# Kernel optimization log

Hardware: AMD Instinct MI355X
Metric: run time of the kernel (lower is better)

Reference implementation:

```python
import jax, jax.numpy as jnp
import numpy as np

N_NODES = 100000
N_EDGES = 600000
F_IN = 128
HIDDEN = 128
Z_DIM = 64


def setup_inputs() -> dict:
    key = jax.random.key(0)
    ks = jax.random.split(key, 8)
    nodes = jax.random.normal(ks[0], (N_NODES, F_IN), dtype=jnp.float32)
    senders = jax.random.randint(ks[1], (N_EDGES,), 0, N_NODES, dtype=jnp.int32)
    receivers = jax.random.randint(ks[2], (N_EDGES,), 0, N_NODES, dtype=jnp.int32)
    s = lambda fan_in: 1.0 / np.sqrt(fan_in)
    W0 = jax.random.normal(ks[3], (F_IN, HIDDEN), dtype=jnp.float32) * s(F_IN)
    b0 = jnp.zeros((HIDDEN,), dtype=jnp.float32)
    W1 = jax.random.normal(ks[4], (HIDDEN, HIDDEN), dtype=jnp.float32) * s(HIDDEN)
    b1 = jnp.zeros((HIDDEN,), dtype=jnp.float32)
    Wmu = jax.random.normal(ks[5], (HIDDEN + F_IN, Z_DIM), dtype=jnp.float32) * s(HIDDEN + F_IN)
    bmu = jnp.zeros((Z_DIM,), dtype=jnp.float32)
    Wls = jax.random.normal(ks[6], (HIDDEN + F_IN, Z_DIM), dtype=jnp.float32) * s(HIDDEN + F_IN)
    bls = jnp.zeros((Z_DIM,), dtype=jnp.float32)
    return dict(nodes=nodes, senders=senders, receivers=receivers,
                W0=W0, b0=b0, W1=W1, b1=b1, Wmu=Wmu, bmu=bmu, Wls=Wls, bls=bls)


def _gc_layer(h, senders, receivers, W, b):
    """jraph.GraphConvolution with symmetric normalization, no self edges.
    update_node_fn = softmax(relu(Dense(h)))."""
    n = h.shape[0]
    h = jax.nn.softmax(jax.nn.relu(h @ W + b), axis=-1)  # [N, H]
    ones = jnp.ones_like(senders, dtype=h.dtype)
    sender_deg = jax.ops.segment_sum(ones, senders, num_segments=n)    # [N]
    receiver_deg = jax.ops.segment_sum(ones, receivers, num_segments=n)
    h = h * jax.lax.rsqrt(jnp.maximum(sender_deg, 1.0))[:, None]
    h = jax.ops.segment_sum(h[senders], receivers, num_segments=n)     # scatter-aggregate
    h = h * jax.lax.rsqrt(jnp.maximum(receiver_deg, 1.0))[:, None]
    return h


def reference(nodes, senders, receivers, W0, b0, W1, b1, Wmu, bmu, Wls, bls):
    h = _gc_layer(nodes, senders, receivers, W0, b0)
    h = _gc_layer(h, senders, receivers, W1, b1)
    h = jnp.concatenate([h, nodes], axis=-1)  # [N, HIDDEN + F_IN]
    mu = h @ Wmu + bmu
    logsig2 = h @ Wls + bls
    return (mu, logsig2)
```

## Files before the change

kernel.cpp:

```cpp
#include <hip/hip_runtime.h>

#define N_NODES 100000
#define N_EDGES 600000

#define NBUCK 391
#define BROWS 512
#define NCHUNK 128
#define V4_TOTAL (N_EDGES / 4)
#define V4_CHUNK ((V4_TOTAL + NCHUNK - 1) / NCHUNK)

typedef __attribute__((ext_vector_type(8))) short short8;
typedef __attribute__((ext_vector_type(4))) float f32x4;

__device__ inline unsigned short bf16r(float x) {
    unsigned u = __float_as_uint(x);
    return (unsigned short)((u + 0x7FFFu + ((u >> 16) & 1u)) >> 16);
}
__device__ inline unsigned bf16pack2(float x, float y) {
    unsigned ux = __float_as_uint(x), uy = __float_as_uint(y);
    ux = (ux + 0x7FFFu + ((ux >> 16) & 1u)) >> 16;
    uy = (uy + 0x7FFFu + ((uy >> 16) & 1u)) >> 16;
    return ux | (uy << 16);
}

__global__ void prep_weights(const float* __restrict__ W0, const float* __restrict__ W1,
                             const float* __restrict__ Wmu, const float* __restrict__ Wls,
                             unsigned short* __restrict__ w0t, unsigned short* __restrict__ w1t,
                             unsigned short* __restrict__ wht) {
    int i = blockIdx.x * 256 + threadIdx.x;
    if (i < 16384) {
        int nn = i >> 7, k = i & 127;
        w0t[i] = bf16r(W0[k * 128 + nn]);
    } else if (i < 32768) {
        int j = i - 16384;
        int nn = j >> 7, k = j & 127;
        w1t[j] = bf16r(W1[k * 128 + nn]);
    } else {
        int j = i - 32768;
        int nn = j >> 8, k = j & 255;
        float v = (nn < 64) ? Wmu[k * 64 + nn] : Wls[k * 64 + (nn - 64)];
        wht[j] = bf16r(v);
    }
}

__global__ __launch_bounds__(1024)
void bucket_hist(const int* __restrict__ receivers, const int* __restrict__ senders,
                 int* __restrict__ hR, int* __restrict__ hS) {
    __shared__ int cR[BROWS], cS[BROWS];
    const int t = threadIdx.x;
    if (t < BROWS) { cR[t] = 0; cS[t] = 0; }
    __syncthreads();
    const int v0 = blockIdx.x * V4_CHUNK;
    const int v1 = min(v0 + V4_CHUNK, V4_TOTAL);
    for (int i = v0 + t; i < v1; i += 1024) {
        const int4 r = ((const int4*)receivers)[i];
        const int4 s = ((const int4*)senders)[i];
        atomicAdd(&cR[r.x >> 8], 1); atomicAdd(&cR[r.y >> 8], 1);
        atomicAdd(&cR[r.z >> 8], 1); atomicAdd(&cR[r.w >> 8], 1);
        atomicAdd(&cS[s.x >> 8], 1); atomicAdd(&cS[s.y >> 8], 1);
        atomicAdd(&cS[s.z >> 8], 1); atomicAdd(&cS[s.w >> 8], 1);
    }
    __syncthreads();
    if (t < BROWS) {
        hR[blockIdx.x * BROWS + t] = cR[t];
        hS[blockIdx.x * BROWS + t] = cS[t];
    }
}

__global__ __launch_bounds__(512)
void bucket_scan(int* __restrict__ hR, int* __restrict__ hS,
                 int* __restrict__ baseR, int* __restrict__ baseS) {
    __shared__ int a[BROWS], b[BROWS], a2[BROWS], b2[BROWS];
    const int t = threadIdx.x;
    int totR = 0, totS = 0;
    for (int blk = 0; blk < NCHUNK; ++blk) {
        totR += hR[blk * BROWS + t];
        totS += hS[blk * BROWS + t];
    }
    a[t] = totR; a2[t] = totS;
    __syncthreads();
    int* pin = a; int* pout = b; int* qin = a2; int* qout = b2;
    for (int off = 1; off < BROWS; off <<= 1) {
        pout[t] = pin[t] + ((t >= off) ? pin[t - off] : 0);
        qout[t] = qin[t] + ((t >= off) ? qin[t - off] : 0);
        __syncthreads();
        int* tmp = pin; pin = pout; pout = tmp;
        tmp = qin; qin = qout; qout = tmp;
    }
    const int bR = pin[t] - totR;
    const int bS = qin[t] - totS;
    if (t <= NBUCK) { baseR[t] = (t == NBUCK) ? N_EDGES : bR; }
    if (t <= NBUCK) { baseS[t] = (t == NBUCK) ? N_EDGES : bS; }
    int curR = bR, curS = bS;
    for (int blk = 0; blk < NCHUNK; ++blk) {
        const int vR = hR[blk * BROWS + t]; hR[blk * BROWS + t] = curR; curR += vR;
        const int vS = hS[blk * BROWS + t]; hS[blk * BROWS + t] = curS; curS += vS;
    }
}

__global__ __launch_bounds__(1024)
void bucket_scatter(const int* __restrict__ receivers, const int* __restrict__ senders,
                    const int* __restrict__ hR, const int* __restrict__ hS,
                    uint2* __restrict__ pairs, int* __restrict__ sbuf) {
    __shared__ int cR[BROWS], cS[BROWS];
    const int t = threadIdx.x;
    if (t < BROWS) {
        cR[t] = hR[blockIdx.x * BROWS + t];
        cS[t] = hS[blockIdx.x * BROWS + t];
    }
    __syncthreads();
    const int v0 = blockIdx.x * V4_CHUNK;
    const int v1 = min(v0 + V4_CHUNK, V4_TOTAL);
    for (int i = v0 + t; i < v1; i += 1024) {
        const int4 r = ((const int4*)receivers)[i];
        const int4 s = ((const int4*)senders)[i];
        int p;
        p = atomicAdd(&cR[r.x >> 8], 1); pairs[p] = make_uint2((unsigned)r.x, (unsigned)s.x);
        p = atomicAdd(&cR[r.y >> 8], 1); pairs[p] = make_uint2((unsigned)r.y, (unsigned)s.y);
        p = atomicAdd(&cR[r.z >> 8], 1); pairs[p] = make_uint2((unsigned)r.z, (unsigned)s.z);
        p = atomicAdd(&cR[r.w >> 8], 1); pairs[p] = make_uint2((unsigned)r.w, (unsigned)s.w);
        p = atomicAdd(&cS[s.x >> 8], 1); sbuf[p] = s.x;
        p = atomicAdd(&cS[s.y >> 8], 1); sbuf[p] = s.y;
        p = atomicAdd(&cS[s.z >> 8], 1); sbuf[p] = s.z;
        p = atomicAdd(&cS[s.w >> 8], 1); sbuf[p] = s.w;
    }
}

__global__ __launch_bounds__(256)
void bucket_finalize(const uint2* __restrict__ pairs, const int* __restrict__ baseR,
                     int* __restrict__ offs, int* __restrict__ srt,
                     float* __restrict__ inv_r, int n) {
    __shared__ int cnt[256], cur[256];
    __shared__ int sa[256], sb[256];
    const int t = threadIdx.x;
    const int b = blockIdx.x;
    const int e0 = baseR[b], e1 = baseR[b + 1];
    cnt[t] = 0;
    __syncthreads();
    for (int i = e0 + t; i < e1; i += 256)
        atomicAdd(&cnt[pairs[i].x & 255u], 1);
    __syncthreads();
    const int v = cnt[t];
    sa[t] = v;
    __syncthreads();
    int* pin = sa; int* pout = sb;
    for (int off = 1; off < 256; off <<= 1) {
        pout[t] = pin[t] + ((t >= off) ? pin[t - off] : 0);
        __syncthreads();
        int* tmp = pin; pin = pout; pout = tmp;
    }
    cur[t] = pin[t] - v;
    const int node = (b << 8) + t;
    if (node < n) {
        offs[node] = e0 + pin[t] - v;
        inv_r[node] = rsqrtf(fmaxf((float)v, 1.0f));
    }
    if (b == 0 && t == 0) offs[n] = N_EDGES;
    __syncthreads();
    for (int i = e0 + t; i < e1; i += 256) {
        const uint2 pr = pairs[i];
        const int p = atomicAdd(&cur[pr.x & 255u], 1);
        srt[e0 + p] = (int)pr.y;
    }
}

__global__ __launch_bounds__(256)
void sender_count(const int* __restrict__ sbuf, const int* __restrict__ baseS,
                  float* __restrict__ inv_s, int n) {
    __shared__ int cnt[256];
    const int t = threadIdx.x;
    const int b = blockIdx.x;
    const int e0 = baseS[b], e1 = baseS[b + 1];
    cnt[t] = 0;
    __syncthreads();
    for (int i = e0 + t; i < e1; i += 256)
        atomicAdd(&cnt[sbuf[i] & 255], 1);
    __syncthreads();
    const int node = (b << 8) + t;
    if (node < n) inv_s[node] = rsqrtf(fmaxf((float)cnt[t], 1.0f));
}

__global__ __launch_bounds__(256)
void aggregate_kernel(const uint4* __restrict__ src, uint4* __restrict__ dst,
                      const int* __restrict__ offs, const int* __restrict__ srt,
                      const float* __restrict__ scale, int n) {
    const int lane = threadIdx.x & 63;
    const int wave = threadIdx.x >> 6;
    const int grp  = lane >> 4;
    const int l16  = lane & 15;
    const int wid  = blockIdx.x * 4 + wave;
    const int nwv  = gridDim.x * 4;
    const unsigned grpbase = lane & 48;

    for (int rb = wid * 4; rb < n; rb += nwv * 4) {
        const int r = rb + grp;
        const bool valid = (r < n);
        int beg = 0, deg = 0;
        if (valid) { beg = offs[r]; deg = offs[r + 1] - beg; }
        float ax[8];
        #pragma unroll
        for (int k = 0; k < 8; ++k) ax[k] = 0.0f;

        for (int j0 = 0; ; j0 += 16) {
            const int rem = deg - j0;
            int wm = rem;
            wm = max(wm, __shfl_xor(wm, 16));
            wm = max(wm, __shfl_xor(wm, 32));
            if (wm <= 0) break;
            const int idx = (j0 + l16 < deg) ? srt[beg + j0 + l16] : 0;
            const int jmax = (wm < 16) ? wm : 16;
            for (int j = 0; j < jmax; j += 8) {
                uint4 v[8];
                #pragma unroll
                for (int k = 0; k < 8; ++k) {
                    const int s = __shfl(idx, grpbase + j + k);
                    v[k] = make_uint4(0u, 0u, 0u, 0u);
                    if (j + k < rem) v[k] = src[(size_t)s * 16 + l16];
                }
                #pragma unroll
                for (int k = 0; k < 8; ++k) {
                    ax[0] += __uint_as_float(v[k].x << 16);
                    ax[1] += __uint_as_float(v[k].x & 0xFFFF0000u);
                    ax[2] += __uint_as_float(v[k].y << 16);
                    ax[3] += __uint_as_float(v[k].y & 0xFFFF0000u);
                    ax[4] += __uint_as_float(v[k].z << 16);
                    ax[5] += __uint_as_float(v[k].z & 0xFFFF0000u);
                    ax[6] += __uint_as_float(v[k].w << 16);
                    ax[7] += __uint_as_float(v[k].w & 0xFFFF0000u);
                }
            }
        }
        if (valid) {
            const float sc = scale[r];
            uint4 o;
            o.x = bf16pack2(ax[0] * sc, ax[1] * sc);
            o.y = bf16pack2(ax[2] * sc, ax[3] * sc);
            o.z = bf16pack2(ax[4] * sc, ax[5] * sc);
            o.w = bf16pack2(ax[6] * sc, ax[7] * sc);
            dst[(size_t)r * 16 + l16] = o;
        }
    }
}

template<bool IN_BF16>
__global__ __launch_bounds__(256)
void gc_mfma(const void* __restrict__ xv, const unsigned short* __restrict__ Wt,
             const float* __restrict__ bias, const float* __restrict__ inv_out,
             unsigned short* __restrict__ y, int nrows) {
    __shared__ unsigned short Wl[128 * 136];
    __shared__ float sinv[64];
    const int row0 = blockIdx.x * 64;

    const int lane = threadIdx.x & 63;
    const int w = threadIdx.x >> 6;
    const int q = lane >> 4;
    const int l16 = lane & 15;
    const int grow = row0 + w * 16 + l16;
    const bool rv = (grow < nrows);

    short8 af[4];
    if (IN_BF16) {
        const unsigned short* x = (const unsigned short*)xv;
        #pragma unroll
        for (int k0 = 0; k0 < 4; ++k0) {
            short8 z = {0, 0, 0, 0, 0, 0, 0, 0};
            if (rv) z = *(const short8*)&x[(size_t)grow * 128 + k0 * 32 + q * 8];
            af[k0] = z;
        }
    } else {
        const float* x = (const float*)xv;
        #pragma unroll
        for (int k0 = 0; k0 < 4; ++k0) {
            float4 a = make_float4(0.f, 0.f, 0.f, 0.f);
            float4 b = make_float4(0.f, 0.f, 0.f, 0.f);
            if (rv) {
                a = *(const float4*)&x[(size_t)grow * 128 + k0 * 32 + q * 8];
                b = *(const float4*)&x[(size_t)grow * 128 + k0 * 32 + q * 8 + 4];
            }
            uint4 u = make_uint4(bf16pack2(a.x, a.y), bf16pack2(a.z, a.w),
                                 bf16pack2(b.x, b.y), bf16pack2(b.z, b.w));
            af[k0] = *(short8*)&u;
        }
    }

    if (threadIdx.x < 64) {
        int g = row0 + threadIdx.x;
        sinv[threadIdx.x] = (g < nrows) ? inv_out[g] : 1.0f;
    }

    for (int i = threadIdx.x; i < 128 * 16; i += 256) {
        int r = i >> 4, c = i & 15;
        *(uint4*)&Wl[r * 136 + c * 8] = *(const uint4*)&Wt[r * 128 + c * 8];
    }
    __syncthreads();

    f32x4 acc[8] = {};
    #pragma unroll
    for (int nt = 0; nt < 8; ++nt) {
        #pragma unroll
        for (int k0 = 0; k0 < 4; ++k0) {
            short8 b = *(const short8*)&Wl[(nt * 16 + l16) * 136 + k0 * 32 + q * 8];
            acc[nt] = __builtin_amdgcn_mfma_f32_16x16x32_bf16(af[k0], b, acc[nt], 0, 0, 0);
        }
    }

    float e[8][4];
    float s[4] = {0.f, 0.f, 0.f, 0.f};
    #pragma unroll
    for (int nt = 0; nt < 8; ++nt) {
        const float bv = bias[nt * 16 + l16];
        #pragma unroll
        for (int r = 0; r < 4; ++r) {
            float ev = __expf(fmaxf(acc[nt][r] + bv, 0.0f));
            e[nt][r] = ev;
            s[r] += ev;
        }
    }
    #pragma unroll
    for (int off = 1; off < 16; off <<= 1)
        #pragma unroll
        for (int r = 0; r < 4; ++r)
            s[r] += __shfl_xor(s[r], off);

    __syncthreads();

    #pragma unroll
    for (int r = 0; r < 4; ++r) {
        const int rl = w * 16 + q * 4 + r;
        const float sc = sinv[rl] / s[r];
        #pragma unroll
        for (int nt = 0; nt < 8; ++nt)
            Wl[rl * 136 + nt * 16 + l16] = bf16r(e[nt][r] * sc);
    }
    __syncthreads();

    for (int c = threadIdx.x; c < 64 * 16; c += 256) {
        int r = c >> 4, cu = c & 15;
        int g = row0 + r;
        if (g < nrows) {
            uint4 vv = *(const uint4*)&Wl[r * 136 + cu * 8];
            *(uint4*)&y[(size_t)g * 128 + cu * 8] = vv;
        }
    }
}

__global__ __launch_bounds__(256)
void head_mfma(const unsigned short* __restrict__ h, const float* __restrict__ nodes,
               const unsigned short* __restrict__ Wt,
               const float* __restrict__ bmu, const float* __restrict__ bls,
               float* __restrict__ out, int nrows) {
    __shared__ unsigned short Xl[64 * 264];
    const int row0 = blockIdx.x * 64;
    {
        const uint2* hs = (const uint2*)h;
        for (int c = threadIdx.x; c < 64 * 32; c += 256) {
            int r = c >> 5, cu = c & 31;
            int grow = row0 + r;
            uint2 v = make_uint2(0u, 0u);
            if (grow < nrows) v = hs[(size_t)grow * 32 + cu];
            *((uint2*)&Xl[r * 264] + cu) = v;
        }
    }
    for (int c = threadIdx.x; c < 64 * 32; c += 256) {
        int r = c >> 5, c4 = c & 31;
        int grow = row0 + r;
        float4 v = make_float4(0.f, 0.f, 0.f, 0.f);
        if (grow < nrows) v = *(const float4*)&nodes[(size_t)grow * 128 + c4 * 4];
        *(uint2*)&Xl[r * 264 + 128 + c4 * 4] = make_uint2(bf16pack2(v.x, v.y), bf16pack2(v.z, v.w));
    }
    __syncthreads();

    const int lane = threadIdx.x & 63;
    const int w = threadIdx.x >> 6;
    const int q = lane >> 4;
    const int l16 = lane & 15;

    short8 bf[8][2];
    #pragma unroll
    for (int k0 = 0; k0 < 8; ++k0)
        #pragma unroll
        for (int nt = 0; nt < 2; ++nt) {
            int ncol = w * 32 + nt * 16 + l16;
            bf[k0][nt] = *(const short8*)&Wt[ncol * 256 + k0 * 32 + q * 8];
        }

    f32x4 acc[4][2] = {};
    #pragma unroll
    for (int k0 = 0; k0 < 8; ++k0) {
        #pragma unroll
        for (int m = 0; m < 4; ++m) {
            short8 a = *(const short8*)&Xl[(m * 16 + l16) * 264 + k0 * 32 + q * 8];
            acc[m][0] = __builtin_amdgcn_mfma_f32_16x16x32_bf16(a, bf[k0][0], acc[m][0], 0, 0, 0);
            acc[m][1] = __builtin_amdgcn_mfma_f32_16x16x32_bf16(a, bf[k0][1], acc[m][1], 0, 0, 0);
        }
    }

    const float* bb = (w < 2) ? bmu : bls;
    float* ob = (w < 2) ? out : out + (size_t)nrows * 64;
    const int c0 = (w & 1) * 32 + l16;
    const int c1 = c0 + 16;
    const float b0v = bb[c0], b1v = bb[c1];
    #pragma unroll
    for (int m = 0; m < 4; ++m)
        #pragma unroll
        for (int r = 0; r < 4; ++r) {
            int grow = row0 + m * 16 + q * 4 + r;
            if (grow < nrows) {
                ob[(size_t)grow * 64 + c0] = acc[m][0][r] + b0v;
                ob[(size_t)grow * 64 + c1] = acc[m][1][r] + b1v;
            }
        }
}

extern "C" void kernel_launch(void* const* d_in, const int* in_sizes, int n_in,
                              void* d_out, int out_size, void* d_ws, size_t ws_size,
                              hipStream_t stream) {
    const float* nodes     = (const float*)d_in[0];
    const int*   senders   = (const int*)d_in[1];
    const int*   receivers = (const int*)d_in[2];
    const float* W0  = (const float*)d_in[3];
    const float* b0  = (const float*)d_in[4];
    const float* W1  = (const float*)d_in[5];
    const float* b1  = (const float*)d_in[6];
    const float* Wmu = (const float*)d_in[7];
    const float* bmu = (const float*)d_in[8];
    const float* Wls = (const float*)d_in[9];
    const float* bls = (const float*)d_in[10];
    float* out = (float*)d_out;

    const int N = N_NODES;
    const int NT64 = (N + 63) / 64;

    float* inv_s = (float*)d_ws;
    float* inv_r = inv_s + N;
    unsigned short* buf0 = (unsigned short*)(inv_r + N);
    unsigned short* buf1 = buf0 + (size_t)N * 128;
    unsigned short* w0t  = buf1 + (size_t)N * 128;
    unsigned short* w1t  = w0t + 128 * 128;
    unsigned short* wht  = w1t + 128 * 128;

    int* offs = (int*)d_out;
    int* srt  = offs + (N + 1);

    uint2* pairs = (uint2*)buf0;
    int* sbuf  = (int*)(pairs + N_EDGES);
    int* hR    = sbuf + N_EDGES;
    int* hS    = hR + NCHUNK * BROWS;
    int* baseR = hS + NCHUNK * BROWS;
    int* baseS = baseR + 512;

    prep_weights<<<256, 256, 0, stream>>>(W0, W1, Wmu, Wls, w0t, w1t, wht);

    bucket_hist<<<NCHUNK, 1024, 0, stream>>>(receivers, senders, hR, hS);
    bucket_scan<<<1, 512, 0, stream>>>(hR, hS, baseR, baseS);
    bucket_scatter<<<NCHUNK, 1024, 0, stream>>>(receivers, senders, hR, hS, pairs, sbuf);
    bucket_finalize<<<NBUCK, 256, 0, stream>>>(pairs, baseR, offs, srt, inv_r, N);
    sender_count<<<NBUCK, 256, 0, stream>>>(sbuf, baseS, inv_s, N);

    gc_mfma<false><<<NT64, 256, 0, stream>>>(nodes, w0t, b0, inv_s, buf0, N);
    aggregate_kernel<<<2048, 256, 0, stream>>>((const uint4*)buf0, (uint4*)buf1,
                                               offs, srt, inv_r, N);

    gc_mfma<true><<<NT64, 256, 0, stream>>>(buf1, w1t, b1, inv_s, buf0, N);
    aggregate_kernel<<<2048, 256, 0, stream>>>((const uint4*)buf0, (uint4*)buf1,
                                               offs, srt, inv_r, N);

    head_mfma<<<NT64, 256, 0, stream>>>(buf1, nodes, wht, bmu, bls, out, N);
}
```

Measured before the change: 277.0 us.

## Restructure head MFMA kernel: activations in registers, weights staged in LDS

The head kernel now has each wave load its 16 rows of h and nodes directly from global memory into A-fragment registers, with the fp32-to-bf16 conversion done in registers. The full 128x256 bf16 weight matrix is staged in LDS and read as B fragments. Each wave computes all 128 output columns for its 16 rows, replacing the old split where each wave computed 32 columns for all 64 rows. This removes the LDS round trip for activations, but each block must now copy 64KB of weights into LDS, which raises LDS usage and may lower occupancy.

```diff
diff --git a/kernel.cpp b/kernel.cpp
--- a/kernel.cpp
+++ b/kernel.cpp
@@ -349,67 +349,72 @@
                const unsigned short* __restrict__ Wt,
                const float* __restrict__ bmu, const float* __restrict__ bls,
                float* __restrict__ out, int nrows) {
-    __shared__ unsigned short Xl[64 * 264];
+    __shared__ unsigned short Wl[128 * 264];
     const int row0 = blockIdx.x * 64;
-    {
-        const uint2* hs = (const uint2*)h;
-        for (int c = threadIdx.x; c < 64 * 32; c += 256) {
-            int r = c >> 5, cu = c & 31;
-            int grow = row0 + r;
-            uint2 v = make_uint2(0u, 0u);
-            if (grow < nrows) v = hs[(size_t)grow * 32 + cu];
-            *((uint2*)&Xl[r * 264] + cu) = v;
-        }
-    }
-    for (int c = threadIdx.x; c < 64 * 32; c += 256) {
-        int r = c >> 5, c4 = c & 31;
-        int grow = row0 + r;
-        float4 v = make_float4(0.f, 0.f, 0.f, 0.f);
-        if (grow < nrows) v = *(const float4*)&nodes[(size_t)grow * 128 + c4 * 4];
-        *(uint2*)&Xl[r * 264 + 128 + c4 * 4] = make_uint2(bf16pack2(v.x, v.y), bf16pack2(v.z, v.w));
-    }
-    __syncthreads();
 
     const int lane = threadIdx.x & 63;
     const int w = threadIdx.x >> 6;
     const int q = lane >> 4;
     const int l16 = lane & 15;
-
-    short8 bf[8][2];
-    #pragma unroll
-    for (int k0 = 0; k0 < 8; ++k0)
-        #pragma unroll
-        for (int nt = 0; nt < 2; ++nt) {
-            int ncol = w * 32 + nt * 16 + l16;
-            bf[k0][nt] = *(const short8*)&Wt[ncol * 256 + k0 * 32 + q * 8];
-        }
-
-    f32x4 acc[4][2] = {};
-    #pragma unroll
-    for (int k0 = 0; k0 < 8; ++k0) {
-        #pragma unroll
-        for (int m = 0; m < 4; ++m) {
-            short8 a = *(const short8*)&Xl[(m * 16 + l16) * 264 + k0 * 32 + q * 8];
-            acc[m][0] = __builtin_amdgcn_mfma_f32_16x16x32_bf16(a, bf[k0][0], acc[m][0], 0, 0, 0);
-            acc[m][1] = __builtin_amdgcn_mfma_f32_16x16x32_bf16(a, bf[k0][1], acc[m][1], 0, 0, 0);
-        }
-    }
-
-    const float* bb = (w < 2) ? bmu : bls;
-    float* ob = (w < 2) ? out : out + (size_t)nrows * 64;
-    const int c0 = (w & 1) * 32 + l16;
-    const int c1 = c0 + 16;
-    const float b0v = bb[c0], b1v = bb[c1];
-    #pragma unroll
-    for (int m = 0; m < 4; ++m)
-        #pragma unroll
-        for (int r = 0; r < 4; ++r) {
-            int grow = row0 + m * 16 + q * 4 + r;
-            if (grow < nrows) {
-                ob[(size_t)grow * 64 + c0] = acc[m][0][r] + b0v;
-                ob[(size_t)grow * 64 + c1] = acc[m][1][r] + b1v;
-            }
-        }
+    const int grow = row0 + w * 16 + l16;
+    const bool rv = (grow < nrows);
+
+    short8 af[8];
+    #pragma unroll
+    for (int k0 = 0; k0 < 4; ++k0) {
+        short8 z = {0, 0, 0, 0, 0, 0, 0, 0};
+        if (rv) z = *(const short8*)&h[(size_t)grow * 128 + k0 * 32 + q * 8];
+        af[k0] = z;
+    }
+    #pragma unroll
+    for (int k0 = 0; k0 < 4; ++k0) {
+        float4 a = make_float4(0.f, 0.f, 0.f, 0.f);
+        float4 b = make_float4(0.f, 0.f, 0.f, 0.f);
+        if (rv) {
+            a = *(const float4*)&nodes[(size_t)grow * 128 + k0 * 32 + q * 8];
+            b = *(const float4*)&nodes[(size_t)grow * 128 + k0 * 32 + q * 8 + 4];
+        }
+        uint4 u = make_uint4(bf16pack2(a.x, a.y), bf16pack2(a.z, a.w),
+                             bf16pack2(b.x, b.y), bf16pack2(b.z, b.w));
+        af[4 + k0] = *(short8*)&u;
+    }
+
+    for (int i = threadIdx.x; i < 128 * 32; i += 256) {
+        int r = i >> 5, c = i & 31;
+        *(uint4*)&Wl[r * 264 + c * 8] = *(const uint4*)&Wt[r * 256 + c * 8];
+    }
+    __syncthreads();
+
+    f32x4 acc[8] = {};
+    #pragma unroll
+    for (int nt = 0; nt < 8; ++nt) {
+        #pragma unroll
+        for (int k0 = 0; k0 < 8; ++k0) {
+            short8 b = *(const short8*)&Wl[(nt * 16 + l16) * 264 + k0 * 32 + q * 8];
+            acc[nt] = __builtin_amdgcn_mfma_f32_16x16x32_bf16(af[k0], b, acc[nt], 0, 0, 0);
+        }
+    }
+
+    float bv[8];
+    #pragma unroll
+    for (int nt = 0; nt < 4; ++nt) bv[nt] = bmu[nt * 16 + l16];
+    #pragma unroll
+    for (int nt = 4; nt < 8; ++nt) bv[nt] = bls[(nt - 4) * 16 + l16];
+
+    float* const omu = out;
+    float* const ols = out + (size_t)nrows * 64;
+    #pragma unroll
+    for (int r = 0; r < 4; ++r) {
+        const int g = row0 + w * 16 + q * 4 + r;
+        if (g < nrows) {
+            #pragma unroll
+            for (int nt = 0; nt < 4; ++nt)
+                omu[(size_t)g * 64 + nt * 16 + l16] = acc[nt][r] + bv[nt];
+            #pragma unroll
+            for (int nt = 4; nt < 8; ++nt)
+                ols[(size_t)g * 64 + (nt - 4) * 16 + l16] = acc[nt][r] + bv[nt];
+        }
+    }
 }
 
 extern "C" void kernel_launch(void* const* d_in, const int* in_sizes, int n_in,
```

After: 286.7 us. +3.5%, slower.
